# Optimization experiments

Hardware: AMD Instinct MI355X
Metric: run time of the kernel (lower is better)

## Reference

```python
import jax, jax.numpy as jnp
import numpy as np

GROUP_SIZE = 16
MIN_SIGMA = 1e-4


def setup_inputs() -> dict:
    key = jax.random.key(0)
    k1, k2, k3 = jax.random.split(key, 3)
    B, N, M, F = 4, 8192, 4096, 64
    return {
        "point_cloud": jax.random.normal(k1, (B, 3, N), dtype=jnp.float32),
        "query_cloud": jax.random.normal(k2, (B, 3, M), dtype=jnp.float32),
        "point_features": jax.random.normal(k3, (B, F, N), dtype=jnp.float32),
        "temperature": jnp.asarray(1.0, dtype=jnp.float32),
    }


def reference(point_cloud, query_cloud, point_features, temperature):
    # point_cloud: (B,3,N), query_cloud: (B,3,M), point_features: (B,F,N)
    k = GROUP_SIZE
    # Pairwise squared distances (B, M, N): ||q||^2 + ||p||^2 - 2 q.p
    q_sq = jnp.sum(query_cloud ** 2, axis=1)              # (B, M)
    p_sq = jnp.sum(point_cloud ** 2, axis=1)              # (B, N)
    qp = jnp.einsum('bdm,bdn->bmn', query_cloud, point_cloud)
    d2 = q_sq[:, :, None] + p_sq[:, None, :] - 2.0 * qp   # (B, M, N)
    # k nearest neighbors per query
    _, idx = jax.lax.top_k(-d2, k)                         # (B, M, k)

    # Gather neighbor coords and features: (B, 3, M, k), (B, F, M, k)
    idx_b = idx[:, None, :, :]                             # (B,1,M,k)
    grouped_points = jnp.take_along_axis(
        point_cloud[:, :, None, :], jnp.broadcast_to(idx_b, (idx.shape[0], 3, idx.shape[1], k)), axis=3)
    grouped_features = jnp.take_along_axis(
        point_features[:, :, None, :],
        jnp.broadcast_to(idx_b, (idx.shape[0], point_features.shape[1], idx.shape[1], k)), axis=3)

    # Soft-projection weights
    sigma = jnp.maximum(temperature ** 2, jnp.asarray(MIN_SIGMA, dtype=temperature.dtype))
    deltas = grouped_points - query_cloud[:, :, :, None]   # (B,3,M,k)
    dist = jnp.sum(deltas ** 2, axis=1, keepdims=True) / sigma  # (B,1,M,k)
    weights = jax.nn.softmax(-dist, axis=3)                # (B,1,M,k)

    projected_points = jnp.sum(grouped_points * weights, axis=3)     # (B,3,M)
    propagated_features = jnp.sum(grouped_features * weights, axis=3)  # (B,F,M)
    return (projected_points, propagated_features)
```

## Files before the change

kernel.cpp:

```cpp
#include <hip/hip_runtime.h>


#define BB 4
#define NN 8192
#define MM 4096
#define FF 64
#define KK 16
#define CHUNK 2048
#define NCHUNK 4
#define QPW 4
#define QPB 32
#define SCAP 54
#define NTHR 1024
#define STG 33

__device__ __forceinline__ float min3f(float a, float b, float c) {
    float d;
    asm("v_min3_f32 %0, %1, %2, %3" : "=v"(d) : "v"(a), "v"(b), "v"(c));
    return d;
}

__global__ __launch_bounds__(256) void transpose_feat(const float* __restrict__ pf,
                                                      float* __restrict__ pfT) {
    __shared__ float tile[64][65];
    const int b = blockIdx.y;
    const int n0 = blockIdx.x * 64;
    const int t = threadIdx.x;
    const int n = t & 63, fq = t >> 6;
#pragma unroll
    for (int i = 0; i < 16; ++i) {
        int f = fq * 16 + i;
        tile[f][n] = pf[(size_t)b * FF * NN + (size_t)f * NN + n0 + n];
    }
    __syncthreads();
    const int f2 = t & 63, nq = t >> 6;
#pragma unroll
    for (int i = 0; i < 16; ++i) {
        int nn2 = nq * 16 + i;
        pfT[(size_t)b * NN * FF + (size_t)(n0 + nn2) * FF + f2] = tile[f2][nn2];
    }
}

__device__ __forceinline__ unsigned mapf(float f) {
    unsigned u = __float_as_uint(f);
    return (u & 0x80000000u) ? ~u : (u | 0x80000000u);
}
__device__ __forceinline__ float unmapf(unsigned k) {
    return (k & 0x80000000u) ? __uint_as_float(k ^ 0x80000000u)
                             : __uint_as_float(~k);
}

#define STAGE(C)                                                            \
    do {                                                                    \
        if (t < CHUNK / 4) {                                                \
            int base_ = (C)*CHUNK + t * 4;                                  \
            float4 x4_ = *(const float4*)(pcb + base_);                     \
            float4 y4_ = *(const float4*)(pcb + NN + base_);                \
            float4 z4_ = *(const float4*)(pcb + 2 * NN + base_);            \
            *(float4*)(s_pts + t * 4) = x4_;                                \
            *(float4*)(s_pts + CHUNK + t * 4) = y4_;                        \
            *(float4*)(s_pts + 2 * CHUNK + t * 4) = z4_;                    \
            float4 p4_;                                                     \
            p4_.x = fmaf(x4_.x, x4_.x, fmaf(y4_.x, y4_.x, z4_.x * z4_.x));  \
            p4_.y = fmaf(x4_.y, x4_.y, fmaf(y4_.y, y4_.y, z4_.y * z4_.y));  \
            p4_.z = fmaf(x4_.z, x4_.z, fmaf(y4_.z, y4_.z, z4_.z * z4_.z));  \
            p4_.w = fmaf(x4_.w, x4_.w, fmaf(y4_.w, y4_.w, z4_.w * z4_.w));  \
            *(float4*)(s_pts + 3 * CHUNK + t * 4) = p4_;                    \
        }                                                                   \
    } while (0)

#define VAL(X, Y, Z, PS, Q) \
    fmaf((X), qx2[Q], fmaf((Y), qy2[Q], fmaf((Z), qz2[Q], (PS))))

#define PUSH(WQ, V, I)                                          \
    do {                                                        \
        int pos_ = atomicAdd(&s_cnt[WQ], 1);                    \
        if (pos_ < SCAP) {                                      \
            s_surv[((WQ)*SCAP + pos_) * 2] = (V);               \
            s_surv[((WQ)*SCAP + pos_) * 2 + 1] = __int_as_float(I); \
        }                                                       \
    } while (0)

__global__ __launch_bounds__(NTHR, 8) void soft_proj_kernel(
    const float* __restrict__ pc, const float* __restrict__ qc,
    const float* __restrict__ pf, const float* __restrict__ pfT,
    const float* __restrict__ temp, float* __restrict__ out, int useT) {
    __shared__ __align__(16) float s_pts[4 * CHUNK];
    __shared__ __align__(16) float s_surv[QPB * SCAP * 2];
    __shared__ int s_cnt[QPB];
    __shared__ int s_sel[QPB * KK];
    __shared__ float s_thr[2 * QPB];

    const int bid = blockIdx.x;
    const int b = bid >> 7;
    const int m0 = (bid & 127) * QPB;
    const int t = threadIdx.x;
    const int wave = t >> 6;
    const int lane = t & 63;
    const int pairIdx = wave & 7;
    const int half = wave >> 3;

    const float* pcb = pc + (size_t)b * 3 * NN;
    const float* qcb = qc + (size_t)b * 3 * MM;

    float qx2[QPW], qy2[QPW], qz2[QPW];
#pragma unroll
    for (int q = 0; q < QPW; ++q) {
        int m = m0 + pairIdx * QPW + q;
        qx2[q] = -2.0f * qcb[m];
        qy2[q] = -2.0f * qcb[MM + m];
        qz2[q] = -2.0f * qcb[2 * MM + m];
    }

    float mnA[QPW], mnB[QPW];
#pragma unroll
    for (int q = 0; q < QPW; ++q) { mnA[q] = 3.0e38f; mnB[q] = 3.0e38f; }

    for (int c = 0; c < NCHUNK; ++c) {
        __syncthreads();
        STAGE(c);
        __syncthreads();
        const int ob = half * 1024 + lane * 4;
#pragma unroll
        for (int g = 0; g < 4; ++g) {
            int oo = ob + g * 256;
            float4 x4 = *(const float4*)(s_pts + oo);
            float4 y4 = *(const float4*)(s_pts + CHUNK + oo);
            float4 z4 = *(const float4*)(s_pts + 2 * CHUNK + oo);
            float4 p4 = *(const float4*)(s_pts + 3 * CHUNK + oo);
#pragma unroll
            for (int q = 0; q < QPW; ++q) {
                float v0 = VAL(x4.x, y4.x, z4.x, p4.x, q);
                float v1 = VAL(x4.y, y4.y, z4.y, p4.y, q);
                float v2 = VAL(x4.z, y4.z, z4.z, p4.z, q);
                float v3 = VAL(x4.w, y4.w, z4.w, p4.w, q);
                mnA[q] = min3f(v0, v1, mnA[q]);
                mnB[q] = min3f(v2, v3, mnB[q]);
            }
        }
    }

    float thrv[QPW];
#pragma unroll
    for (int q = 0; q < QPW; ++q) {
        unsigned key = mapf(fminf(mnA[q], mnB[q]));
        unsigned res = 0u;
        for (int bb = 31; bb >= 16; --bb) {
            unsigned cand = res | (1u << bb);
            unsigned long long bal = __ballot(key < cand);
            int c2 = __popcll(bal);
            if (c2 < 8) res = cand;
        }
        thrv[q] = unmapf(res | 0xFFFFu);
    }
    if (lane == 0) {
#pragma unroll
        for (int q = 0; q < QPW; ++q)
            s_thr[half * QPB + pairIdx * QPW + q] = thrv[q];
    }
    if (t < QPB) s_cnt[t] = 0;
    __syncthreads();
#pragma unroll
    for (int q = 0; q < QPW; ++q)
        thrv[q] = fmaxf(s_thr[pairIdx * QPW + q], s_thr[QPB + pairIdx * QPW + q]);

    for (int c = 0; c < NCHUNK; ++c) {
        __syncthreads();
        STAGE(c);
        __syncthreads();
        const int ob = half * 1024 + lane * 4;
#pragma unroll
        for (int g = 0; g < 4; ++g) {
            int oo = ob + g * 256;
            float4 x4 = *(const float4*)(s_pts + oo);
            float4 y4 = *(const float4*)(s_pts + CHUNK + oo);
            float4 z4 = *(const float4*)(s_pts + 2 * CHUNK + oo);
            float4 p4 = *(const float4*)(s_pts + 3 * CHUNK + oo);
            int gi = c * CHUNK + oo;
#pragma unroll
            for (int q = 0; q < QPW; ++q) {
                float v0 = VAL(x4.x, y4.x, z4.x, p4.x, q);
                float v1 = VAL(x4.y, y4.y, z4.y, p4.y, q);
                float v2 = VAL(x4.z, y4.z, z4.z, p4.z, q);
                float v3 = VAL(x4.w, y4.w, z4.w, p4.w, q);
                if (fminf(min3f(v0, v1, v2), v3) <= thrv[q]) {
                    int wqq = pairIdx * QPW + q;
                    if (v0 <= thrv[q]) PUSH(wqq, v0, gi + 0);
                    if (v1 <= thrv[q]) PUSH(wqq, v1, gi + 1);
                    if (v2 <= thrv[q]) PUSH(wqq, v2, gi + 2);
                    if (v3 <= thrv[q]) PUSH(wqq, v3, gi + 3);
                }
            }
        }
    }
    __syncthreads();

#pragma unroll
    for (int qq = 0; qq < 2; ++qq) {
        int wq = wave * 2 + qq;
        int cnt = s_cnt[wq];
        cnt = __builtin_amdgcn_readfirstlane(cnt);
        if (cnt > SCAP) cnt = SCAP;
        bool valid = lane < cnt;
        float mv = 0.f;
        int mi = 0;
        if (valid) {
            mv = s_surv[(wq * SCAP + lane) * 2];
            mi = __float_as_int(s_surv[(wq * SCAP + lane) * 2 + 1]);
        }
        int rank = 0;
        for (int j = 0; j < cnt; ++j) {
            float vj = s_surv[(wq * SCAP + j) * 2];
            int ij = __float_as_int(s_surv[(wq * SCAP + j) * 2 + 1]);
            if (valid && (vj < mv || (vj == mv && ij < mi))) rank++;
        }
        if (valid && rank < KK) s_sel[wq * KK + rank] = mi;
    }
    __syncthreads();

    float* stage = s_surv;
    float tval = temp[0];
    float sigma = fmaxf(tval * tval, 1.0e-4f);
    float inv_sigma = 1.0f / sigma;
    const float* pfTb = pfT + (size_t)b * NN * FF;
    const float* pfb = pf + (size_t)b * FF * NN;

#pragma unroll
    for (int qq = 0; qq < 2; ++qq) {
        int wq = wave * 2 + qq;
        int m = m0 + wq;
        float qxe = qcb[m], qye = qcb[MM + m], qze = qcb[2 * MM + m];
        int ik = s_sel[wq * KK + (lane & 15)];
        float px = pcb[ik], py = pcb[NN + ik], pz = pcb[2 * NN + ik];
        float dx = px - qxe, dy = py - qye, dz = pz - qze;
        float dk = fmaf(dx, dx, fmaf(dy, dy, dz * dz));
        float dmin = dk;
#pragma unroll
        for (int s = 1; s < 16; s <<= 1) dmin = fminf(dmin, __shfl_xor(dmin, s));
        float e = __expf((dmin - dk) * inv_sigma);
        float ssum = e;
#pragma unroll
        for (int s = 1; s < 16; s <<= 1) ssum += __shfl_xor(ssum, s);
        float w = e * (1.0f / ssum);
        float sx = w * px, sy = w * py, sz = w * pz;
#pragma unroll
        for (int s = 1; s < 16; s <<= 1) {
            sx += __shfl_xor(sx, s);
            sy += __shfl_xor(sy, s);
            sz += __shfl_xor(sz, s);
        }
        float facc = 0.f;
#pragma unroll
        for (int k = 0; k < KK; ++k) {
            float wk = __shfl(w, k);
            int iik = __shfl(ik, k);
            float fv = useT ? pfTb[(size_t)iik * FF + lane]
                            : pfb[(size_t)lane * NN + iik];
            facc = fmaf(wk, fv, facc);
        }
        stage[lane * STG + wq] = facc;
        if (lane == 0) {
            stage[(64) * STG + wq] = sx;
            stage[(65) * STG + wq] = sy;
            stage[(66) * STG + wq] = sz;
        }
    }
    __syncthreads();

    const size_t featOff = (size_t)BB * 3 * MM;
    for (int j = t; j < 67 * QPB; j += NTHR) {
        int row = j >> 5, col = j & 31;
        float v = stage[row * STG + col];
        int m = m0 + col;
        if (row < 64)
            out[featOff + (size_t)b * FF * MM + (size_t)row * MM + m] = v;
        else
            out[(size_t)b * 3 * MM + (size_t)(row - 64) * MM + m] = v;
    }
}

extern "C" void kernel_launch(void* const* d_in, const int* in_sizes, int n_in,
                              void* d_out, int out_size, void* d_ws, size_t ws_size,
                              hipStream_t stream) {
    (void)in_sizes; (void)n_in; (void)out_size;
    const float* pc = (const float*)d_in[0];
    const float* qc = (const float*)d_in[1];
    const float* pf = (const float*)d_in[2];
    const float* temp = (const float*)d_in[3];
    float* out = (float*)d_out;
    float* pfT = (float*)d_ws;
    const size_t needT = (size_t)BB * NN * FF * sizeof(float);
    int useT = (ws_size >= needT && d_ws != nullptr) ? 1 : 0;

    if (useT) {
        hipLaunchKernelGGL(transpose_feat, dim3(NN / 64, BB), dim3(256), 0, stream,
                           pf, pfT);
    }
    hipLaunchKernelGGL(soft_proj_kernel, dim3((BB * MM) / QPB), dim3(NTHR), 0,
                       stream, pc, qc, pf, pfT, temp, out, useT);
}
```

Baseline: 118.9 us.

## Remap second-pass work so each wave handles 8 queries over a quarter chunk

In the survivor-collection pass, each wave now covers 8 queries across a quarter of the staged chunk instead of 4 queries across half of it. Query coordinates are reloaded from global memory, and thresholds are read from shared memory per the new mapping. Each shared-memory point load is now reused across twice as many queries, which cuts LDS traffic per distance computation. The cost is more registers per thread and more atomics contending on the same survivor counters.

```diff
diff --git a/kernel.cpp b/kernel.cpp
--- a/kernel.cpp
+++ b/kernel.cpp
@@ -69,8 +69,8 @@
         }                                                                   \
     } while (0)
 
-#define VAL(X, Y, Z, PS, Q) \
-    fmaf((X), qx2[Q], fmaf((Y), qy2[Q], fmaf((Z), qz2[Q], (PS))))
+#define VAL(X, Y, Z, PS, QX, QY, QZ) \
+    fmaf((X), (QX), fmaf((Y), (QY), fmaf((Z), (QZ), (PS))))
 
 #define PUSH(WQ, V, I)                                          \
     do {                                                        \
@@ -130,17 +130,16 @@
             float4 p4 = *(const float4*)(s_pts + 3 * CHUNK + oo);
 #pragma unroll
             for (int q = 0; q < QPW; ++q) {
-                float v0 = VAL(x4.x, y4.x, z4.x, p4.x, q);
-                float v1 = VAL(x4.y, y4.y, z4.y, p4.y, q);
-                float v2 = VAL(x4.z, y4.z, z4.z, p4.z, q);
-                float v3 = VAL(x4.w, y4.w, z4.w, p4.w, q);
+                float v0 = VAL(x4.x, y4.x, z4.x, p4.x, qx2[q], qy2[q], qz2[q]);
+                float v1 = VAL(x4.y, y4.y, z4.y, p4.y, qx2[q], qy2[q], qz2[q]);
+                float v2 = VAL(x4.z, y4.z, z4.z, p4.z, qx2[q], qy2[q], qz2[q]);
+                float v3 = VAL(x4.w, y4.w, z4.w, p4.w, qx2[q], qy2[q], qz2[q]);
                 mnA[q] = min3f(v0, v1, mnA[q]);
                 mnB[q] = min3f(v2, v3, mnB[q]);
             }
         }
     }
 
-    float thrv[QPW];
 #pragma unroll
     for (int q = 0; q < QPW; ++q) {
         unsigned key = mapf(fminf(mnA[q], mnB[q]));
@@ -151,26 +150,31 @@
             int c2 = __popcll(bal);
             if (c2 < 8) res = cand;
         }
-        thrv[q] = unmapf(res | 0xFFFFu);
-    }
-    if (lane == 0) {
-#pragma unroll
-        for (int q = 0; q < QPW; ++q)
-            s_thr[half * QPB + pairIdx * QPW + q] = thrv[q];
+        if (lane == 0)
+            s_thr[half * QPB + pairIdx * QPW + q] = unmapf(res | 0xFFFFu);
     }
     if (t < QPB) s_cnt[t] = 0;
     __syncthreads();
-#pragma unroll
-    for (int q = 0; q < QPW; ++q)
-        thrv[q] = fmaxf(s_thr[pairIdx * QPW + q], s_thr[QPB + pairIdx * QPW + q]);
+
+    const int qo = (wave >> 2) * 8;
+    const int qtr = wave & 3;
+    float qx2b[8], qy2b[8], qz2b[8], thv[8];
+#pragma unroll
+    for (int q = 0; q < 8; ++q) {
+        int m = m0 + qo + q;
+        qx2b[q] = -2.0f * qcb[m];
+        qy2b[q] = -2.0f * qcb[MM + m];
+        qz2b[q] = -2.0f * qcb[2 * MM + m];
+        thv[q] = fmaxf(s_thr[qo + q], s_thr[QPB + qo + q]);
+    }
 
     for (int c = 0; c < NCHUNK; ++c) {
         __syncthreads();
         STAGE(c);
         __syncthreads();
-        const int ob = half * 1024 + lane * 4;
-#pragma unroll
-        for (int g = 0; g < 4; ++g) {
+        const int ob = qtr * 512 + lane * 4;
+#pragma unroll
+        for (int g = 0; g < 2; ++g) {
             int oo = ob + g * 256;
             float4 x4 = *(const float4*)(s_pts + oo);
             float4 y4 = *(const float4*)(s_pts + CHUNK + oo);
@@ -178,17 +182,17 @@
             float4 p4 = *(const float4*)(s_pts + 3 * CHUNK + oo);
             int gi = c * CHUNK + oo;
 #pragma unroll
-            for (int q = 0; q < QPW; ++q) {
-                float v0 = VAL(x4.x, y4.x, z4.x, p4.x, q);
-                float v1 = VAL(x4.y, y4.y, z4.y, p4.y, q);
-                float v2 = VAL(x4.z, y4.z, z4.z, p4.z, q);
-                float v3 = VAL(x4.w, y4.w, z4.w, p4.w, q);
-                if (fminf(min3f(v0, v1, v2), v3) <= thrv[q]) {
-                    int wqq = pairIdx * QPW + q;
-                    if (v0 <= thrv[q]) PUSH(wqq, v0, gi + 0);
-                    if (v1 <= thrv[q]) PUSH(wqq, v1, gi + 1);
-                    if (v2 <= thrv[q]) PUSH(wqq, v2, gi + 2);
-                    if (v3 <= thrv[q]) PUSH(wqq, v3, gi + 3);
+            for (int q = 0; q < 8; ++q) {
+                float v0 = VAL(x4.x, y4.x, z4.x, p4.x, qx2b[q], qy2b[q], qz2b[q]);
+                float v1 = VAL(x4.y, y4.y, z4.y, p4.y, qx2b[q], qy2b[q], qz2b[q]);
+                float v2 = VAL(x4.z, y4.z, z4.z, p4.z, qx2b[q], qy2b[q], qz2b[q]);
+                float v3 = VAL(x4.w, y4.w, z4.w, p4.w, qx2b[q], qy2b[q], qz2b[q]);
+                if (fminf(min3f(v0, v1, v2), v3) <= thv[q]) {
+                    int wqq = qo + q;
+                    if (v0 <= thv[q]) PUSH(wqq, v0, gi + 0);
+                    if (v1 <= thv[q]) PUSH(wqq, v1, gi + 1);
+                    if (v2 <= thv[q]) PUSH(wqq, v2, gi + 2);
+                    if (v3 <= thv[q]) PUSH(wqq, v3, gi + 3);
                 }
             }
         }
```

After: 137.0 us. 15.2% more time.
